# Kernel optimization log

Hardware: AMD Instinct MI355X
Metric: run time of the kernel (lower is better)

## Reference

```python
import jax, jax.numpy as jnp
import numpy as np
from jax import lax

N, E, C, B, EF = 50000, 640000, 128, 64, 2
L = 32            # eval mode: 8 * num_virtual_tokens
D = 256           # mamba d_inner = expand * d_model
S = 128           # mamba d_state
R = 8             # dt_rank = ceil(C/16)
K = 4             # mamba d_conv


def _ln(x, g, b, eps=1e-5):
    m = x.mean(-1, keepdims=True)
    v = jnp.mean((x - m) ** 2, -1, keepdims=True)
    return (x - m) * lax.rsqrt(v + eps) * g + b


def setup_inputs() -> dict:
    key = jax.random.key(0)
    ks = iter(jax.random.split(key, 64))
    nrm = lambda sh, s=0.02: jax.random.normal(next(ks), sh, dtype=jnp.float32) * s
    inp = {}
    inp['x'] = jax.random.normal(next(ks), (N, C), dtype=jnp.float32)
    inp['edge_attr'] = jax.random.normal(next(ks), (E, EF), dtype=jnp.float32)
    inp['edge_index'] = jax.random.randint(next(ks), (2, E), 0, N, dtype=jnp.int32)
    inp['batch'] = jnp.sort(jax.random.randint(next(ks), (N,), 0, B, dtype=jnp.int32))
    # 8 spatial convs: edge-feature lift + node linear
    inp['We'] = nrm((8, EF, C), 0.1); inp['be'] = jnp.zeros((8, C))
    inp['Wc'] = nrm((8, C, C));       inp['bc'] = jnp.zeros((8, C))
    # GRUCell (torch gate order r,z,n)
    inp['Wih'] = nrm((C, 3 * C), 0.05); inp['Whh'] = nrm((C, 3 * C), 0.05)
    inp['bih'] = jnp.zeros((3 * C,));   inp['bhh'] = jnp.zeros((3 * C,))
    # Mamba
    inp['Win'] = nrm((C, 2 * D))
    inp['conv_w'] = nrm((D, K), 0.1); inp['conv_b'] = jnp.zeros((D,))
    inp['Wx'] = nrm((D, R + 2 * S))
    inp['Wdt'] = nrm((R, D), 0.1); inp['bdt'] = jnp.full((D,), -2.0)
    inp['A_log'] = jnp.log(jnp.tile(jnp.arange(1, S + 1, dtype=jnp.float32), (D, 1)))
    inp['Dp'] = jnp.ones((D,))
    inp['Wout'] = nrm((D, C))
    inp['g_m'] = jnp.ones((C,)); inp['b_m'] = jnp.zeros((C,))
    # merge MLP: Linear(9C->C) -> LN -> ReLU -> Linear(C->C)
    inp['Wm1'] = nrm((9 * C, C)); inp['bm1'] = jnp.zeros((C,))
    inp['g_h'] = jnp.ones((C,));  inp['b_h'] = jnp.zeros((C,))
    inp['Wm2'] = nrm((C, C));     inp['bm2'] = jnp.zeros((C,))
    inp['g_o'] = jnp.ones((C,));  inp['b_o'] = jnp.zeros((C,))
    return inp


def _forward(x, edge_attr, We, be, Wc, bc, Wih, Whh, bih, bhh, Win, conv_w, conv_b,
             Wx, Wdt, bdt, A_log, Dp, Wout, g_m, b_m, Wm1, bm1, g_h, b_h, Wm2, bm2,
             g_o, b_o, edge_index, batch):
    src, dst = edge_index[0], edge_index[1]
    # --- 8 graph convs (gather -> edge message -> scatter-add -> linear) ---
    xs = []
    x_src = x[src]                                        # [E,C]
    for i in range(8):
        msg = jax.nn.relu(x_src + edge_attr @ We[i] + be[i])
        agg = jax.ops.segment_sum(msg, dst, num_segments=N)
        xs.append(jax.nn.relu(agg @ Wc[i] + bc[i]))
    # --- to_dense_batch mean (zero-padded mean => segment_sum / maxN) ---
    counts = jax.ops.segment_sum(jnp.ones((N,), x.dtype), batch, num_segments=B)
    maxN = counts.max()
    x_mean = jax.ops.segment_sum(x, batch, num_segments=B) / maxN   # [B,C]
    # --- GRU virtual-token loop (input constant across steps) ---
    gi = x_mean @ Wih + bih
    ir, iz, inn = jnp.split(gi, 3, axis=-1)
    def gru_step(h, _):
        gh = h @ Whh + bhh
        hr, hz, hn = jnp.split(gh, 3, axis=-1)
        r = jax.nn.sigmoid(ir + hr)
        z = jax.nn.sigmoid(iz + hz)
        n = jnp.tanh(inn + r * hn)
        h = (1.0 - z) * n + z * h
        return h, h
    _, toks = lax.scan(gru_step, jnp.zeros((B, C), x.dtype), None, length=L)
    tokens = jnp.moveaxis(toks, 0, 1)                     # [B,L,C]
    # --- Mamba selective scan ---
    xz = tokens @ Win                                     # [B,L,2D]
    x_in, z_g = jnp.split(xz, 2, axis=-1)
    xp = jnp.pad(x_in, ((0, 0), (K - 1, 0), (0, 0)))      # causal depthwise conv
    x_c = sum(conv_w[:, k] * xp[:, k:k + L, :] for k in range(K)) + conv_b
    x_c = jax.nn.silu(x_c)                                # [B,L,D]
    dbl = x_c @ Wx
    dt_r, Bp, Cp = dbl[..., :R], dbl[..., R:R + S], dbl[..., R + S:]
    dt = jax.nn.softplus(dt_r @ Wdt + bdt)                # [B,L,D]
    A = -jnp.exp(A_log)                                   # [D,S]
    def ssm_step(h, inp):
        dt_t, B_t, C_t, x_t = inp                         # [B,D],[B,S],[B,S],[B,D]
        dA = jnp.exp(dt_t[..., None] * A)                 # [B,D,S]
        h = dA * h + (dt_t * x_t)[..., None] * B_t[:, None, :]
        y = jnp.einsum('bds,bs->bd', h, C_t)
        return h, y
    tm = lambda a: jnp.moveaxis(a, 1, 0)
    _, ys = lax.scan(ssm_step, jnp.zeros((B, D, S), x.dtype),
                     (tm(dt), tm(Bp), tm(Cp), tm(x_c)))
    y = jnp.moveaxis(ys, 0, 1) + Dp * x_c
    y = y * jax.nn.silu(z_g)
    mo = _ln(y @ Wout, g_m, b_m)                          # [B,L,C]
    x_m = mo[:, -1, :]
    x_m_node = x_m[batch]                                 # [N,C] gather
    # --- merge + residual + LN ---
    cat = jnp.concatenate(xs + [x_m_node], axis=-1)       # [N,9C]
    h1 = jax.nn.relu(_ln(cat @ Wm1 + bm1, g_h, b_h))
    x_new = h1 @ Wm2 + bm2
    return _ln(x + x_new, g_o, b_o)


def reference(x, edge_index, edge_attr, batch, We, be, Wc, bc, Wih, Whh, bih, bhh,
              Win, conv_w, conv_b, Wx, Wdt, bdt, A_log, Dp, Wout, g_m, b_m,
              Wm1, bm1, g_h, b_h, Wm2, bm2, g_o, b_o):
    return _forward(x, edge_attr, We, be, Wc, bc, Wih, Whh, bih, bhh, Win, conv_w,
                    conv_b, Wx, Wdt, bdt, A_log, Dp, Wout, g_m, b_m, Wm1, bm1,
                    g_h, b_h, Wm2, bm2, g_o, b_o, edge_index, batch)
```

## Files before the change

kernel.cpp:

```cpp
#include <hip/hip_runtime.h>
#include <hip/hip_bf16.h>

#define N_NODES 50000
#define N_EDGES 640000
#define C_DIM 128
#define B_DIM 64
#define L_DIM 32
#define D_DIM 256
#define S_DIM 128
#define R_DIM 8
#define K_CONV 4
#define NPW 4
#define NB 64
#define MAX_CHUNK 50048
#define SCAN_BLK 49

typedef unsigned short u16;
typedef __attribute__((ext_vector_type(8))) short bf16x8;
typedef __attribute__((ext_vector_type(4))) float f32x4;

struct __align__(16) ERec { int s; float a0, a1; int pad; };

__device__ __forceinline__ float bu2f(u16 u){ return __uint_as_float(((unsigned)u) << 16); }
__device__ __forceinline__ u16 f2bu(float f){
  __hip_bfloat16 h = __float2bfloat16(f);
  return *reinterpret_cast<u16*>(&h);
}
__device__ __forceinline__ float sigmoidf_(float x){ return 1.f/(1.f + expf(-x)); }
__device__ __forceinline__ int clampi(int v, int lo, int hi){ return max(lo, min(v, hi)); }
__device__ __forceinline__ float ldf(const void* p, size_t i, int f){
  return f ? bu2f(((const u16*)p)[i]) : ((const float*)p)[i];
}
__device__ __forceinline__ void stf(void* p, size_t i, int f, float v){
  if (f) ((u16*)p)[i] = f2bu(v); else ((float*)p)[i] = v;
}
__device__ __forceinline__ f32x4 mfma16(bf16x8 a, bf16x8 b, f32x4 c){
  return __builtin_amdgcn_mfma_f32_16x16x32_bf16(a, b, c, 0, 0, 0);
}
__device__ __forceinline__ float wave_sum64(float v){
  #pragma unroll
  for (int off = 32; off; off >>= 1) v += __shfl_xor(v, off);
  return v;
}

constexpr int K_SEG = 27;
constexpr int kCum[K_SEG+1] = {
  0, 2048, 3072, 134144, 135168, 184320, 233472, 233856, 234240, 299776,
  300800, 301056, 368640, 370688, 370944, 403712, 403968, 436736, 436864,
  436992, 584448, 584576, 584704, 584832, 601216, 601344, 601472, 601600 };
#define ARENA_TOTAL 601600

struct Ptrs { const void* p[K_SEG]; };


__global__ void detect_kernel(const unsigned* dp_bits, const unsigned* cand1,
                              const unsigned* cand2, int* flags){
  int lane = threadIdx.x & 63;
  unsigned idx = (unsigned)((lane * 9973u) % (unsigned)N_EDGES);
  int v1 = (cand1[idx] < (unsigned)N_NODES) ? 1 : 0;
  int v2 = (cand2[idx] < (unsigned)N_NODES) ? 1 : 0;
  unsigned long long m1 = __ballot(v1);
  unsigned long long m2 = __ballot(v2);
  if (lane == 0){
    flags[0] = (dp_bits[0] == 0x3F803F80u) ? 1 : 0;
    flags[1] = (__popcll(m1) > __popcll(m2)) ? 1 : 0;
  }
}


__global__ __launch_bounds__(256) void cvt_all_kernel(Ptrs ptrs, float* arena,
                                                      const int* flags){
  int i = blockIdx.x*256 + threadIdx.x;
  if (i >= ARENA_TOTAL) return;
  int lo = 0, hi = K_SEG;
  #pragma unroll
  for (int it = 0; it < 5; it++){
    int mid = (lo + hi) >> 1;
    if (i >= kCum[mid]) lo = mid; else hi = mid;
  }
  int elem = i - kCum[lo];
  const void* sp = ptrs.p[lo];
  arena[i] = flags[0] ? bu2f(((const u16*)sp)[elem]) : ((const float*)sp)[elem];
}


__global__ __launch_bounds__(256) void wtrans_kernel(
    const float* __restrict__ WcF, const float* __restrict__ Wm1F,
    const float* __restrict__ Wm2F,
    u16* __restrict__ WcT_hi, u16* __restrict__ WcT_lo,
    u16* __restrict__ Wm1T_hi, u16* __restrict__ Wm1T_lo,
    u16* __restrict__ Wm2T_hi, u16* __restrict__ Wm2T_lo)
{
  int i = blockIdx.x*256 + threadIdx.x;
  if (i >= 8*C_DIM*C_DIM) return;
  int h = i >> 14, j = (i >> 7) & 127, k = i & 127;
  {
    float w = WcF[(h<<14) + (k<<7) + j];
    u16 hi = f2bu(w); u16 lo = f2bu(w - bu2f(hi));
    WcT_hi[i] = hi; WcT_lo[i] = lo;
  }
  {
    float w = Wm1F[((size_t)((h<<7) + k) << 7) + j];
    u16 hi = f2bu(w); u16 lo = f2bu(w - bu2f(hi));
    Wm1T_hi[i] = hi; Wm1T_lo[i] = lo;
  }
  if (i < C_DIM*C_DIM){
    int j2 = i >> 7, k2 = i & 127;
    float w = Wm2F[(k2<<7) + j2];
    u16 hi = f2bu(w); u16 lo = f2bu(w - bu2f(hi));
    Wm2T_hi[i] = hi; Wm2T_lo[i] = lo;
  }
}


__global__ void hist_kernel(const int* __restrict__ eiA, const int* __restrict__ eiB,
                            const int* __restrict__ flags, int* __restrict__ hist){
  const int* dst = (flags[1] ? eiA : eiB) + N_EDGES;
  int e = blockIdx.x*256 + threadIdx.x;
  if (e >= N_EDGES) return;
  int d = clampi(dst[e], 0, N_NODES-1);
  atomicAdd(&hist[d], 1);
}

__global__ __launch_bounds__(1024) void scan1_kernel(const int* __restrict__ hist,
                                                     int* __restrict__ tmp,
                                                     int* __restrict__ bsums){
  __shared__ int buf[1024];
  int b = blockIdx.x, tid = threadIdx.x;
  int i = b*1024 + tid;
  int v = (i < N_NODES) ? hist[i] : 0;
  buf[tid] = v;
  __syncthreads();
  for (int off = 1; off < 1024; off <<= 1){
    int t = (tid >= off) ? buf[tid-off] : 0;
    __syncthreads();
    buf[tid] += t;
    __syncthreads();
  }
  if (i < N_NODES) tmp[i] = buf[tid];
  if (tid == 1023) bsums[b] = buf[1023];
}

__global__ void scan2_kernel(int* __restrict__ bsums, int* __restrict__ offsets){
  if (threadIdx.x == 0){
    int run = 0;
    for (int b = 0; b < SCAN_BLK; b++){ int v = bsums[b]; bsums[b] = run; run += v; }
    offsets[N_NODES] = run;
  }
}

__global__ __launch_bounds__(1024) void scan3_kernel(int* __restrict__ offsets,
                                                     int* __restrict__ hist,
                                                     const int* __restrict__ bsums){
  int b = blockIdx.x, tid = threadIdx.x;
  int i = b*1024 + tid;
  if (i >= N_NODES) return;
  int incl = offsets[i];
  int h = hist[i];
  int excl = incl - h + bsums[b];
  offsets[i] = excl;
  hist[i] = excl;
}

__global__ void perm_kernel(const void* __restrict__ in1, const void* __restrict__ in2,
                            const int* __restrict__ flags, int* __restrict__ cursor,
                            ERec* __restrict__ sortedRec){
  int e = blockIdx.x*256 + threadIdx.x;
  if (e >= N_EDGES) return;
  const int f1 = flags[1], f = flags[0];
  const int* ei  = (const int*)(f1 ? in1 : in2);
  const void* eav = f1 ? in2 : in1;
  int d = clampi(ei[N_EDGES + e], 0, N_NODES-1);
  int s = clampi(ei[e], 0, N_NODES-1);
  float a0, a1;
  if (f){ const u16* e16 = (const u16*)eav; a0 = bu2f(e16[2*e]); a1 = bu2f(e16[2*e+1]); }
  else  { const float* e32 = (const float*)eav; a0 = e32[2*e]; a1 = e32[2*e+1]; }
  int pos = atomicAdd(&cursor[d], 1);
  pos = clampi(pos, 0, N_EDGES-1);
  ERec r; r.s = s; r.a0 = a0; r.a1 = a1; r.pad = 0;
  sortedRec[pos] = r;
}


__global__ __launch_bounds__(256, 8) void gather_kernel(
    const void* __restrict__ xv, const ERec* __restrict__ sortedRec,
    const int* __restrict__ offsets,
    const float* __restrict__ WeF, const float* __restrict__ beF,
    const int* __restrict__ flags, u16* __restrict__ aggBuf,
    int n0, int ncnt)
{
  int w = blockIdx.x*4 + (threadIdx.x >> 6);
  int nsets = (ncnt + NPW - 1) / NPW;
  if (w >= 2*nsets) return;
  int chalf = w & 1;
  int nset = w >> 1;
  int lane = threadIdx.x & 63;
  int c = lane + chalf*64;
  const int f = flags[0];
  const u16* x16 = (const u16*)xv; const float* x32 = (const float*)xv;

  float we0[8], we1[8], beh[8];
  #pragma unroll
  for (int h = 0; h < 8; h++){
    we0[h] = WeF[h*2*C_DIM + c];
    we1[h] = WeF[h*2*C_DIM + C_DIM + c];
    beh[h] = beF[h*C_DIM + c];
  }

  auto LD = [&](int q, float& xr, float2& er){
    ERec r = sortedRec[q];
    er = make_float2(r.a0, r.a1);
    int idx = r.s*C_DIM + c;
    xr = f ? bu2f(x16[idx]) : x32[idx];
  };

  int nl_end = min(nset*NPW + NPW, ncnt);
  for (int nl = nset*NPW; nl < nl_end; nl++){
    int n = n0 + nl;
    int q0 = offsets[n];
    int cnt = offsets[n+1] - q0;

    float acc[8] = {0,0,0,0,0,0,0,0};
    float xA=0.f, xB=0.f, xC=0.f, xD=0.f;
    float2 eA=make_float2(0,0), eB=make_float2(0,0), eC=make_float2(0,0), eD=make_float2(0,0);
    if (cnt > 0) LD(q0+0, xA, eA);
    if (cnt > 1) LD(q0+1, xB, eB);
    if (cnt > 2) LD(q0+2, xC, eC);
    if (cnt > 3) LD(q0+3, xD, eD);

    for (int j = 0; j < cnt; j += 4){
      float ux0=xA, ux1=xB, ux2=xC, ux3=xD;
      float2 ue0=eA, ue1=eB, ue2=eC, ue3=eD;
      if (j+4 < cnt) LD(q0+j+4, xA, eA);
      if (j+5 < cnt) LD(q0+j+5, xB, eB);
      if (j+6 < cnt) LD(q0+j+6, xC, eC);
      if (j+7 < cnt) LD(q0+j+7, xD, eD);
      #pragma unroll
      for (int h = 0; h < 8; h++)
        acc[h] += fmaxf(fmaf(ue0.x, we0[h], fmaf(ue0.y, we1[h], ux0 + beh[h])), 0.f);
      if (j+1 < cnt){
        #pragma unroll
        for (int h = 0; h < 8; h++)
          acc[h] += fmaxf(fmaf(ue1.x, we0[h], fmaf(ue1.y, we1[h], ux1 + beh[h])), 0.f);
      }
      if (j+2 < cnt){
        #pragma unroll
        for (int h = 0; h < 8; h++)
          acc[h] += fmaxf(fmaf(ue2.x, we0[h], fmaf(ue2.y, we1[h], ux2 + beh[h])), 0.f);
      }
      if (j+3 < cnt){
        #pragma unroll
        for (int h = 0; h < 8; h++)
          acc[h] += fmaxf(fmaf(ue3.x, we0[h], fmaf(ue3.y, we1[h], ux3 + beh[h])), 0.f);
      }
    }

    int base = nl*2048 + c;
    #pragma unroll
    for (int h = 0; h < 8; h++){
      u16 hv = f2bu(acc[h]);
      u16 lv = f2bu(acc[h] - bu2f(hv));
      aggBuf[base + h*256]       = hv;
      aggBuf[base + h*256 + 128] = lv;
    }
  }
}


__global__ __launch_bounds__(128) void pool_kernel(
    const void* __restrict__ xv, const int* __restrict__ batch,
    float* __restrict__ xsum, int* __restrict__ counts, const int* __restrict__ flags)
{
  int c = threadIdx.x;
  int f = flags[0];
  int n0 = blockIdx.x * 32;
  int nend = min(n0 + 32, N_NODES);
  float acc = 0.f; int cnt = 0;
  int curb = clampi(batch[n0], 0, B_DIM-1);
  for (int n = n0; n < nend; n++){
    int b = clampi(batch[n], 0, B_DIM-1);
    if (b != curb){
      atomicAdd(&xsum[curb*C_DIM + c], acc);
      if (c == 0) atomicAdd(&counts[curb], cnt);
      acc = 0.f; cnt = 0; curb = b;
    }
    acc += ldf(xv, (size_t)n*C_DIM + c, f);
    cnt++;
  }
  atomicAdd(&xsum[curb*C_DIM + c], acc);
  if (c == 0) atomicAdd(&counts[curb], cnt);
}


__global__ __launch_bounds__(384, 1) void gru_kernel(
    const float* __restrict__ xsum, const int* __restrict__ counts,
    const float* __restrict__ Wih, const float* __restrict__ bih,
    const float* __restrict__ Whh, const float* __restrict__ bhh,
    float* __restrict__ tokens)
{
  int b = blockIdx.x, j = threadIdx.x;
  __shared__ float xm[C_DIM], h[C_DIM], gh[3*C_DIM], sgi[3*C_DIM];
  __shared__ float mxS;
  if (j == 0){
    int m = 1;
    for (int bb = 0; bb < B_DIM; bb++) m = max(m, counts[bb]);
    mxS = (float)m;
  }
  __syncthreads();
  if (j < C_DIM){ xm[j] = xsum[b*C_DIM + j] / mxS; h[j] = 0.f; }
  __syncthreads();

  {
    float a0=0.f, a1=0.f, a2=0.f, a3=0.f;
    for (int k = 0; k < C_DIM; k += 4){
      a0 = fmaf(xm[k],   Wih[(k  )*384 + j], a0);
      a1 = fmaf(xm[k+1], Wih[(k+1)*384 + j], a1);
      a2 = fmaf(xm[k+2], Wih[(k+2)*384 + j], a2);
      a3 = fmaf(xm[k+3], Wih[(k+3)*384 + j], a3);
    }
    sgi[j] = bih[j] + ((a0 + a1) + (a2 + a3));
  }

  float w[C_DIM];
  #pragma unroll
  for (int k = 0; k < C_DIM; k++) w[k] = Whh[k*384 + j];
  float bh = bhh[j];
  __syncthreads();

  float g_ir = 0.f, g_iz = 0.f, g_in = 0.f;
  if (j < C_DIM){ g_ir = sgi[j]; g_iz = sgi[C_DIM + j]; g_in = sgi[2*C_DIM + j]; }

  for (int t = 0; t < L_DIM; t++){
    float a0=0.f, a1=0.f, a2=0.f, a3=0.f;
    #pragma unroll
    for (int k = 0; k < C_DIM; k += 4){
      a0 = fmaf(h[k],   w[k],   a0);
      a1 = fmaf(h[k+1], w[k+1], a1);
      a2 = fmaf(h[k+2], w[k+2], a2);
      a3 = fmaf(h[k+3], w[k+3], a3);
    }
    gh[j] = bh + ((a0 + a1) + (a2 + a3));
    __syncthreads();
    if (j < C_DIM){
      float r  = sigmoidf_(g_ir + gh[j]);
      float z  = sigmoidf_(g_iz + gh[C_DIM + j]);
      float nn = tanhf(g_in + r*gh[2*C_DIM + j]);
      float hn = (1.f - z)*nn + z*h[j];
      h[j] = hn;
      tokens[((size_t)b*L_DIM + t)*C_DIM + j] = hn;
    }
    __syncthreads();
  }
}


__global__ __launch_bounds__(256) void token_proj_kernel(
    const float* __restrict__ tokens, const float* __restrict__ Win,
    float* __restrict__ x_in, float* __restrict__ z_last)
{
  int row = blockIdx.x;
  int d = threadIdx.x;
  __shared__ float tok[C_DIM];
  if (d < C_DIM) tok[d] = tokens[(size_t)row*C_DIM + d];
  __syncthreads();
  float acc = 0.f;
  for (int k = 0; k < C_DIM; k++) acc = fmaf(tok[k], Win[k*512 + d], acc);
  x_in[(size_t)row*D_DIM + d] = acc;
  if ((row & (L_DIM-1)) == L_DIM-1){
    float acc2 = 0.f;
    for (int k = 0; k < C_DIM; k++) acc2 = fmaf(tok[k], Win[k*512 + D_DIM + d], acc2);
    z_last[(row >> 5)*D_DIM + d] = acc2;
  }
}


__global__ __launch_bounds__(256) void xproj_kernel(
    const float* __restrict__ x_in, const float* __restrict__ cw,
    const float* __restrict__ cb, const float* __restrict__ Wx,
    const float* __restrict__ Wdt, const float* __restrict__ bdt,
    float* __restrict__ dt, float* __restrict__ Bp, float* __restrict__ Cp,
    float* __restrict__ x_c)
{
  int row = blockIdx.x; int tid = threadIdx.x;
  int t = row & (L_DIM-1);
  __shared__ float xr[D_DIM];
  __shared__ float dtr[R_DIM];
  float acc0 = cb[tid];
  #pragma unroll
  for (int k = 0; k < K_CONV; k++){
    int tt = t + k - (K_CONV-1);
    if (tt >= 0) acc0 = fmaf(cw[tid*K_CONV + k], x_in[(size_t)(row + tt - t)*D_DIM + tid], acc0);
  }
  float xcv = acc0 * sigmoidf_(acc0);
  x_c[(size_t)row*D_DIM + tid] = xcv;
  xr[tid] = xcv;
  __syncthreads();
  float acc = 0.f;
  #pragma unroll 4
  for (int k = 0; k < D_DIM; k++) acc = fmaf(xr[k], Wx[k*264 + tid], acc);
  if (tid < R_DIM)              dtr[tid] = acc;
  else if (tid < R_DIM+S_DIM)   Bp[(size_t)row*S_DIM + tid - R_DIM] = acc;
  else                          Cp[(size_t)row*S_DIM + tid - (R_DIM+S_DIM)] = acc;
  if (tid < 264 - D_DIM){
    float acc2 = 0.f;
    #pragma unroll 4
    for (int k = 0; k < D_DIM; k++) acc2 = fmaf(xr[k], Wx[k*264 + D_DIM + tid], acc2);
    Cp[(size_t)row*S_DIM + (D_DIM - (R_DIM+S_DIM)) + tid] = acc2;
  }
  __syncthreads();
  float a = bdt[tid];
  #pragma unroll
  for (int r = 0; r < R_DIM; r++) a = fmaf(dtr[r], Wdt[r*D_DIM + tid], a);
  dt[(size_t)row*D_DIM + tid] = (a > 20.f) ? a : log1pf(expf(a));
}


__global__ __launch_bounds__(256) void ssm_kernel(
    const float* __restrict__ dt, const float* __restrict__ Bp,
    const float* __restrict__ Cp, const float* __restrict__ x_c,
    const float* __restrict__ A_log, const float* __restrict__ Dp_,
    const float* __restrict__ z_last, float* __restrict__ y_last)
{
  int wid = (blockIdx.x*256 + threadIdx.x) >> 6;
  int lane = threadIdx.x & 63;
  int b = wid >> 8, d = wid & (D_DIM-1);
  int s0 = lane*2;
  float A0 = -expf(A_log[d*S_DIM + s0]);
  float A1 = -expf(A_log[d*S_DIM + s0 + 1]);
  float h0 = 0.f, h1 = 0.f;
  for (int t = 0; t < L_DIM; t++){
    int row = b*L_DIM + t;
    float dtv = dt[(size_t)row*D_DIM + d];
    float xv  = x_c[(size_t)row*D_DIM + d];
    float bx = dtv * xv;
    float2 Bv = ((const float2*)(Bp + (size_t)row*S_DIM))[lane];
    h0 = fmaf(expf(dtv*A0), h0, bx*Bv.x);
    h1 = fmaf(expf(dtv*A1), h1, bx*Bv.y);
  }
  int row = b*L_DIM + (L_DIM-1);
  float2 Cv = ((const float2*)(Cp + (size_t)row*S_DIM))[lane];
  float y = h0*Cv.x + h1*Cv.y;
  #pragma unroll
  for (int off = 32; off; off >>= 1) y += __shfl_down(y, off);
  if (lane == 0){
    float xc = x_c[(size_t)row*D_DIM + d];
    float yv = y + Dp_[d]*xc;
    float z  = z_last[b*D_DIM + d];
    yv *= z * sigmoidf_(z);
    y_last[b*D_DIM + d] = yv;
  }
}


__device__ __forceinline__ float block_sum_128(float v, float* red){
  int c = threadIdx.x;
  red[c] = v; __syncthreads();
  if (c < 64) red[c] += red[c+64];
  __syncthreads();
  if (c < 64){
    float r = red[c];
    #pragma unroll
    for (int off = 32; off; off >>= 1) r += __shfl_down(r, off);
    if (c == 0) red[0] = r;
  }
  __syncthreads();
  float out = red[0];
  __syncthreads();
  return out;
}

__global__ __launch_bounds__(128) void xm_kernel(
    const float* __restrict__ y_last, const float* __restrict__ Wout,
    const float* __restrict__ g_m, const float* __restrict__ b_m,
    const float* __restrict__ Wm1x, float* __restrict__ proj)
{
  int b = blockIdx.x, c = threadIdx.x;
  __shared__ float yr[D_DIM];
  __shared__ float red[C_DIM];
  __shared__ float xmr[C_DIM];
  yr[c]        = y_last[b*D_DIM + c];
  yr[C_DIM+c]  = y_last[b*D_DIM + C_DIM + c];
  __syncthreads();
  float acc = 0.f;
  for (int k = 0; k < D_DIM; k++) acc = fmaf(yr[k], Wout[k*C_DIM + c], acc);
  float mean = block_sum_128(acc, red) * (1.f/C_DIM);
  float dv = acc - mean;
  float var = block_sum_128(dv*dv, red) * (1.f/C_DIM);
  float mo = dv*rsqrtf(var + 1e-5f)*g_m[c] + b_m[c];
  xmr[c] = mo;
  __syncthreads();
  float p = 0.f;
  for (int k = 0; k < C_DIM; k++) p = fmaf(xmr[k], Wm1x[k*C_DIM + c], p);
  proj[b*C_DIM + c] = p;
}


__global__ __launch_bounds__(256, 2) void fused_kernel(
    const void* __restrict__ xv, const u16* __restrict__ aggBuf, int n0, int ncnt,
    const u16* __restrict__ WcT_hi, const u16* __restrict__ WcT_lo,
    const float* __restrict__ bcF,
    const u16* __restrict__ Wm1T_hi, const u16* __restrict__ Wm1T_lo,
    const float* __restrict__ bm1F, const float* __restrict__ proj,
    const int* __restrict__ batch,
    const float* __restrict__ ghF, const float* __restrict__ bhF,
    const u16* __restrict__ Wm2T_hi, const u16* __restrict__ Wm2T_lo,
    const float* __restrict__ bm2F,
    const float* __restrict__ goF, const float* __restrict__ boF,
    const int* __restrict__ flags, void* __restrict__ out)
{
  __shared__ __align__(16) char smem[65536];
  float* pS = (float*)smem;

  const int tid = threadIdx.x;
  const int f = flags[0];
  const u16* x16 = (const u16*)xv; const float* x32 = (const float*)xv;
  const int lbase = blockIdx.x * NB;
  const int nbase = n0 + lbase;

  const int lane = tid & 63;
  const int wv = tid >> 6;
  const int m16 = lane & 15;
  const int lg = lane >> 4;
  const int colbase = wv * 32;
  const int jA = colbase + m16;

  int ahoff[4], aoff[4];
  #pragma unroll
  for (int kk = 0; kk < 4; kk++){
    int sw = (m16 & 7) << 4;
    ahoff[kk] = m16*512 + ((kk*64 + lg*16) ^ sw);
    aoff[kk]  = m16*256 + ((kk*64 + lg*16) ^ sw);
  }

  int sg_node[8], sg_u[8], sg_dst[8];
  #pragma unroll
  for (int j = 0; j < 8; j++){
    int i = tid + j*256;
    int t = i >> 9, g = (i >> 5) & 15, u = i & 31;
    sg_node[j] = lbase + t*16 + g;
    sg_u[j] = u << 4;
    sg_dst[j] = t*8192 + (((i & 511) << 4) ^ ((g & 7) << 4));
  }

  bf16x8 sreg[8];
  auto stage_load = [&](int h){
    #pragma unroll
    for (int j = 0; j < 8; j++)
      sreg[j] = *(const bf16x8*)((const char*)aggBuf +
                 (((size_t)sg_node[j]*8 + h) << 9) + sg_u[j]);
  };
  auto stage_commit = [&](){
    #pragma unroll
    for (int j = 0; j < 8; j++) *(bf16x8*)(smem + sg_dst[j]) = sreg[j];
  };
  auto LDW = [&](const u16* Whi, const u16* Wlo, int h, bf16x8 (*w)[4]){
    #pragma unroll
    for (int kk = 0; kk < 4; kk++){
      size_t bi0 = ((size_t)(h*C_DIM + jA) << 7) + kk*32 + lg*8;
      w[kk][0] = *(const bf16x8*)(Whi + bi0);
      w[kk][1] = *(const bf16x8*)(Wlo + bi0);
      w[kk][2] = *(const bf16x8*)(Whi + bi0 + 2048);
      w[kk][3] = *(const bf16x8*)(Wlo + bi0 + 2048);
    }
  };

  stage_load(0);
  stage_commit();
  __syncthreads();

  f32x4 P0[4], P1[4];
  #pragma unroll
  for (int t = 0; t < 4; t++){
    P0[t] = (f32x4){0,0,0,0};
    P1[t] = (f32x4){0,0,0,0};
  }

  bf16x8 w[4][4];
  for (int h = 0; h < 8; h++){
    const bool pf = (h+1 < 8);
    LDW(WcT_hi, WcT_lo, h, w);
    if (pf) stage_load(h+1);
    float bc0 = bcF[h*C_DIM + colbase + m16];
    float bc1 = bcF[h*C_DIM + colbase + 16 + m16];

    #pragma unroll
    for (int t = 0; t < 4; t++){
      f32x4 a0 = {0,0,0,0}, a1 = {0,0,0,0};
      #pragma unroll
      for (int kk = 0; kk < 4; kk++){
        bf16x8 ah = *(const bf16x8*)(smem + t*8192 + ahoff[kk]);
        bf16x8 al = *(const bf16x8*)(smem + t*8192 + ahoff[kk] + 256);
        a0 = mfma16(ah, w[kk][0], a0);
        a0 = mfma16(ah, w[kk][1], a0);
        a0 = mfma16(al, w[kk][0], a0);
        a1 = mfma16(ah, w[kk][2], a1);
        a1 = mfma16(ah, w[kk][3], a1);
        a1 = mfma16(al, w[kk][2], a1);
      }
      #pragma unroll
      for (int r = 0; r < 4; r++){
        int row = lg*4 + r;
        int rs = row*256;
        int sw2 = (row & 7) << 4;
        {
          float v = fmaxf(a0[r] + bc0, 0.f);
          u16 hi = f2bu(v); u16 lo = f2bu(v - bu2f(hi));
          int bo = rs + (((colbase + m16)*2) ^ sw2);
          *(u16*)(smem + 32768 + t*8192 + bo) = hi;
          *(u16*)(smem + 32768 + t*8192 + 4096 + bo) = lo;
        }
        {
          float v = fmaxf(a1[r] + bc1, 0.f);
          u16 hi = f2bu(v); u16 lo = f2bu(v - bu2f(hi));
          int bo = rs + (((colbase + 16 + m16)*2) ^ sw2);
          *(u16*)(smem + 32768 + t*8192 + bo) = hi;
          *(u16*)(smem + 32768 + t*8192 + 4096 + bo) = lo;
        }
      }
    }
    LDW(Wm1T_hi, Wm1T_lo, h, w);
    __syncthreads();
    if (pf) stage_commit();

    #pragma unroll
    for (int t = 0; t < 4; t++){
      #pragma unroll
      for (int kk = 0; kk < 4; kk++){
        bf16x8 yh = *(const bf16x8*)(smem + 32768 + t*8192 + aoff[kk]);
        bf16x8 yl = *(const bf16x8*)(smem + 32768 + t*8192 + 4096 + aoff[kk]);
        P0[t] = mfma16(yh, w[kk][0], P0[t]);
        P0[t] = mfma16(yh, w[kk][1], P0[t]);
        P0[t] = mfma16(yl, w[kk][0], P0[t]);
        P1[t] = mfma16(yh, w[kk][2], P1[t]);
        P1[t] = mfma16(yh, w[kk][3], P1[t]);
        P1[t] = mfma16(yl, w[kk][2], P1[t]);
      }
    }
    __syncthreads();
  }

  #pragma unroll
  for (int t = 0; t < 4; t++){
    #pragma unroll
    for (int r = 0; r < 4; r++){
      int row = t*16 + lg*4 + r;
      pS[row*C_DIM + colbase + m16]      = P0[t][r];
      pS[row*C_DIM + colbase + 16 + m16] = P1[t][r];
    }
  }
  __syncthreads();

  for (int g = 0; g < 16; g++){
    int n_l = wv*16 + g;
    int nc = min(nbase + n_l, N_NODES-1);
    int bi = clampi(batch[nc], 0, B_DIM-1);
    float v0 = pS[n_l*C_DIM + lane]      + bm1F[lane]      + proj[bi*C_DIM + lane];
    float v1 = pS[n_l*C_DIM + 64 + lane] + bm1F[64 + lane] + proj[bi*C_DIM + 64 + lane];
    float mean = wave_sum64(v0 + v1) * (1.f/C_DIM);
    float d0 = v0 - mean, d1 = v1 - mean;
    float var = wave_sum64(d0*d0 + d1*d1) * (1.f/C_DIM);
    float rinv = rsqrtf(var + 1e-5f);
    float h0 = fmaxf(d0*rinv*ghF[lane]      + bhF[lane], 0.f);
    float h1v = fmaxf(d1*rinv*ghF[64+lane]  + bhF[64+lane], 0.f);
    int sw3 = (n_l & 7) << 4;
    {
      u16 hi = f2bu(h0); u16 lo = f2bu(h0 - bu2f(hi));
      int bo = n_l*256 + ((lane*2) ^ sw3);
      *(u16*)(smem + 32768 + bo) = hi;
      *(u16*)(smem + 49152 + bo) = lo;
    }
    {
      u16 hi = f2bu(h1v); u16 lo = f2bu(h1v - bu2f(hi));
      int bo = n_l*256 + (((64+lane)*2) ^ sw3);
      *(u16*)(smem + 32768 + bo) = hi;
      *(u16*)(smem + 49152 + bo) = lo;
    }
  }
  LDW(Wm2T_hi, Wm2T_lo, 0, w);
  __syncthreads();

  {
    f32x4 A0[4], A1[4];
    #pragma unroll
    for (int t = 0; t < 4; t++){
      A0[t] = (f32x4){0,0,0,0};
      A1[t] = (f32x4){0,0,0,0};
      #pragma unroll
      for (int kk = 0; kk < 4; kk++){
        bf16x8 yh = *(const bf16x8*)(smem + 32768 + t*4096 + aoff[kk]);
        bf16x8 yl = *(const bf16x8*)(smem + 49152 + t*4096 + aoff[kk]);
        A0[t] = mfma16(yh, w[kk][0], A0[t]);
        A0[t] = mfma16(yh, w[kk][1], A0[t]);
        A0[t] = mfma16(yl, w[kk][0], A0[t]);
        A1[t] = mfma16(yh, w[kk][2], A1[t]);
        A1[t] = mfma16(yh, w[kk][3], A1[t]);
        A1[t] = mfma16(yl, w[kk][2], A1[t]);
      }
    }
    __syncthreads();
    #pragma unroll
    for (int t = 0; t < 4; t++){
      #pragma unroll
      for (int r = 0; r < 4; r++){
        int row = t*16 + lg*4 + r;
        pS[row*C_DIM + colbase + m16]      = A0[t][r];
        pS[row*C_DIM + colbase + 16 + m16] = A1[t][r];
      }
    }
  }
  __syncthreads();

  for (int g = 0; g < 16; g++){
    int n_l = wv*16 + g;
    int n = nbase + n_l;
    int nc = min(n, N_NODES-1);
    float x0 = f ? bu2f(x16[(size_t)nc*C_DIM + lane])      : x32[(size_t)nc*C_DIM + lane];
    float x1 = f ? bu2f(x16[(size_t)nc*C_DIM + 64 + lane]) : x32[(size_t)nc*C_DIM + 64 + lane];
    float v0 = pS[n_l*C_DIM + lane]      + bm2F[lane]      + x0;
    float v1 = pS[n_l*C_DIM + 64 + lane] + bm2F[64 + lane] + x1;
    float mean = wave_sum64(v0 + v1) * (1.f/C_DIM);
    float d0 = v0 - mean, d1 = v1 - mean;
    float var = wave_sum64(d0*d0 + d1*d1) * (1.f/C_DIM);
    float rinv = rsqrtf(var + 1e-5f);
    if (lbase + n_l < ncnt){
      stf(out, (size_t)n*C_DIM + lane,      f, d0*rinv*goF[lane]      + boF[lane]);
      stf(out, (size_t)n*C_DIM + 64 + lane, f, d1*rinv*goF[64+lane]   + boF[64+lane]);
    }
  }
}


extern "C" void kernel_launch(void* const* d_in, const int* in_sizes, int n_in,
                              void* d_out, int out_size, void* d_ws, size_t ws_size,
                              hipStream_t stream)
{
  const void* x      = d_in[0];
  const void* in1    = d_in[1];
  const void* in2    = d_in[2];
  const int*  batch  = (const int*)d_in[3];
  (void)in_sizes; (void)n_in; (void)out_size;

  char* ws = (char*)d_ws;
  size_t off = 0;
  auto alloc = [&](size_t nbytes)->char*{
    char* p = ws + off;
    off += (nbytes + 255) & ~(size_t)255;
    return p;
  };
  int*   flags = (int*)alloc(8);
  float* arena = (float*)alloc((size_t)ARENA_TOTAL*4);
  int* hist    = (int*)alloc((size_t)N_NODES*4);
  int* offsets = (int*)alloc((size_t)(N_NODES+1)*4);
  int* bsums   = (int*)alloc((size_t)SCAN_BLK*4);
  ERec* sortedRec = (ERec*)alloc((size_t)N_EDGES*16);
  float* proj   = (float*)alloc((size_t)B_DIM*C_DIM*4);
  float* xsum   = (float*)alloc((size_t)B_DIM*C_DIM*4);
  int*   counts = (int*)alloc((size_t)B_DIM*4);
  float* tokens = (float*)alloc((size_t)B_DIM*L_DIM*C_DIM*4);
  float* x_in   = (float*)alloc((size_t)B_DIM*L_DIM*D_DIM*4);
  float* x_c    = (float*)alloc((size_t)B_DIM*L_DIM*D_DIM*4);
  float* Cp     = (float*)alloc((size_t)B_DIM*L_DIM*S_DIM*4);
  float* z_last = (float*)alloc((size_t)B_DIM*D_DIM*4);
  float* y_last = (float*)alloc((size_t)B_DIM*D_DIM*4);
  u16* WcT_hi  = (u16*)alloc((size_t)8*C_DIM*C_DIM*2);
  u16* WcT_lo  = (u16*)alloc((size_t)8*C_DIM*C_DIM*2);
  u16* Wm1T_hi = (u16*)alloc((size_t)8*C_DIM*C_DIM*2);
  u16* Wm1T_lo = (u16*)alloc((size_t)8*C_DIM*C_DIM*2);
  u16* Wm2T_hi = (u16*)alloc((size_t)C_DIM*C_DIM*2);
  u16* Wm2T_lo = (u16*)alloc((size_t)C_DIM*C_DIM*2);

  size_t avail = (ws_size > off + 4096) ? (ws_size - off - 4096) : 0;
  long long cn = (long long)(avail / 4096);
  cn &= ~63LL;
  if (cn > MAX_CHUNK) cn = MAX_CHUNK;
  if (cn < 64) cn = 16704;
  const int chunkN = (int)cn;
  u16* aggBuf = (u16*)alloc((size_t)chunkN * 4096);

  float* Bp  = tokens;
  float* dtb = x_in;

  float* WeF   = arena + 0;      float* beF   = arena + 2048;
  float* WcF   = arena + 3072;   float* bcF   = arena + 134144;
  float* WihF  = arena + 135168; float* WhhF  = arena + 184320;
  float* bihF  = arena + 233472; float* bhhF  = arena + 233856;
  float* WinF  = arena + 234240; float* cwF   = arena + 299776;
  float* cbF   = arena + 300800; float* WxF   = arena + 301056;
  float* WdtF  = arena + 368640; float* bdtF  = arena + 370688;
  float* AlF   = arena + 370944; float* DpF   = arena + 403712;
  float* WoutF = arena + 403968; float* gmF   = arena + 436736;
  float* bmF   = arena + 436864; float* Wm1F  = arena + 436992;
  float* bm1F  = arena + 584448; float* ghF   = arena + 584576;
  float* bhF   = arena + 584704; float* Wm2F  = arena + 584832;
  float* bm2F  = arena + 601216; float* goF   = arena + 601344;
  float* boF   = arena + 601472;

  detect_kernel<<<1, 64, 0, stream>>>((const unsigned*)d_in[19],
                                      (const unsigned*)in1, (const unsigned*)in2, flags);

  Ptrs ptrs;
  for (int i = 0; i < K_SEG; i++) ptrs.p[i] = d_in[4 + i];
  cvt_all_kernel<<<(ARENA_TOTAL + 255)/256, 256, 0, stream>>>(ptrs, arena, flags);
  wtrans_kernel<<<(8*C_DIM*C_DIM + 255)/256, 256, 0, stream>>>(
      WcF, Wm1F, Wm2F, WcT_hi, WcT_lo, Wm1T_hi, Wm1T_lo, Wm2T_hi, Wm2T_lo);

  hipMemsetAsync(hist, 0, (size_t)N_NODES*4, stream);
  hist_kernel<<<(N_EDGES + 255)/256, 256, 0, stream>>>((const int*)in1, (const int*)in2, flags, hist);
  scan1_kernel<<<SCAN_BLK, 1024, 0, stream>>>(hist, offsets, bsums);
  scan2_kernel<<<1, 64, 0, stream>>>(bsums, offsets);
  scan3_kernel<<<SCAN_BLK, 1024, 0, stream>>>(offsets, hist, bsums);
  perm_kernel<<<(N_EDGES + 255)/256, 256, 0, stream>>>(in1, in2, flags, hist, sortedRec);

  hipMemsetAsync(xsum, 0, (size_t)B_DIM*C_DIM*4 + 256, stream);
  pool_kernel<<<(N_NODES + 31)/32, 128, 0, stream>>>(x, batch, xsum, counts, flags);
  gru_kernel<<<B_DIM, 384, 0, stream>>>(xsum, counts, WihF, bihF, WhhF, bhhF, tokens);
  token_proj_kernel<<<B_DIM*L_DIM, 256, 0, stream>>>(tokens, WinF, x_in, z_last);
  xproj_kernel<<<B_DIM*L_DIM, 256, 0, stream>>>(x_in, cwF, cbF, WxF, WdtF, bdtF, dtb, Bp, Cp, x_c);
  ssm_kernel<<<(B_DIM*D_DIM)/4, 256, 0, stream>>>(dtb, Bp, Cp, x_c, AlF, DpF, z_last, y_last);
  xm_kernel<<<B_DIM, 128, 0, stream>>>(y_last, WoutF, gmF, bmF, Wm1F + 8*C_DIM*C_DIM, proj);

  for (int n0 = 0; n0 < N_NODES; n0 += chunkN){
    int ncnt = min(chunkN, N_NODES - n0);
    int nsets = (ncnt + NPW - 1) / NPW;
    int nwaves = 2 * nsets;
    gather_kernel<<<(nwaves + 3)/4, 256, 0, stream>>>(
        x, sortedRec, offsets, WeF, beF, flags, aggBuf, n0, ncnt);
    fused_kernel<<<(ncnt + NB - 1)/NB, 256, 0, stream>>>(
        x, aggBuf, n0, ncnt, WcT_hi, WcT_lo, bcF, Wm1T_hi, Wm1T_lo, bm1F,
        proj, batch, ghF, bhF, Wm2T_hi, Wm2T_lo, bm2F, goF, boF, flags, d_out);
  }
}
```

Before: 796.6 us.

## Shrink fused kernel LDS to raise occupancy, load aggregates straight from global

The fused conv+merge kernel drops LDS staging of the aggregated neighbor features. MFMA A-operands now load directly from global memory, and the per-node LayerNorm epilogues run in 16-row slices that use a small scratch region. This cuts shared memory from 64 KiB to 40 KiB and raises the launch-bounds occupancy target from 2 to 3 blocks per CU. In exchange the A loads lose the swizzled, software-prefetched LDS path, are less coalesced and are exposed to global latency, and the slice epilogues add barriers.

```diff
diff --git a/kernel.cpp b/kernel.cpp
--- a/kernel.cpp
+++ b/kernel.cpp
@@ -495,7 +495,7 @@
 }
 
 
-__global__ __launch_bounds__(256, 2) void fused_kernel(
+__global__ __launch_bounds__(256, 3) void fused_kernel(
     const void* __restrict__ xv, const u16* __restrict__ aggBuf, int n0, int ncnt,
     const u16* __restrict__ WcT_hi, const u16* __restrict__ WcT_lo,
     const float* __restrict__ bcF,
@@ -508,8 +508,8 @@
     const float* __restrict__ goF, const float* __restrict__ boF,
     const int* __restrict__ flags, void* __restrict__ out)
 {
-  __shared__ __align__(16) char smem[65536];
-  float* pS = (float*)smem;
+  __shared__ __align__(16) char smem[40960];
+  float* pS = (float*)(smem + 32768);
 
   const int tid = threadIdx.x;
   const int f = flags[0];
@@ -524,35 +524,13 @@
   const int colbase = wv * 32;
   const int jA = colbase + m16;
 
-  int ahoff[4], aoff[4];
+  int aoff[4];
   #pragma unroll
   for (int kk = 0; kk < 4; kk++){
     int sw = (m16 & 7) << 4;
-    ahoff[kk] = m16*512 + ((kk*64 + lg*16) ^ sw);
-    aoff[kk]  = m16*256 + ((kk*64 + lg*16) ^ sw);
-  }
-
-  int sg_node[8], sg_u[8], sg_dst[8];
-  #pragma unroll
-  for (int j = 0; j < 8; j++){
-    int i = tid + j*256;
-    int t = i >> 9, g = (i >> 5) & 15, u = i & 31;
-    sg_node[j] = lbase + t*16 + g;
-    sg_u[j] = u << 4;
-    sg_dst[j] = t*8192 + (((i & 511) << 4) ^ ((g & 7) << 4));
-  }
-
-  bf16x8 sreg[8];
-  auto stage_load = [&](int h){
-    #pragma unroll
-    for (int j = 0; j < 8; j++)
-      sreg[j] = *(const bf16x8*)((const char*)aggBuf +
-                 (((size_t)sg_node[j]*8 + h) << 9) + sg_u[j]);
-  };
-  auto stage_commit = [&](){
-    #pragma unroll
-    for (int j = 0; j < 8; j++) *(bf16x8*)(smem + sg_dst[j]) = sreg[j];
-  };
+    aoff[kk] = m16*256 + ((kk*64 + lg*16) ^ sw);
+  }
+
   auto LDW = [&](const u16* Whi, const u16* Wlo, int h, bf16x8 (*w)[4]){
     #pragma unroll
     for (int kk = 0; kk < 4; kk++){
@@ -564,10 +542,6 @@
     }
   };
 
-  stage_load(0);
-  stage_commit();
-  __syncthreads();
-
   f32x4 P0[4], P1[4];
   #pragma unroll
   for (int t = 0; t < 4; t++){
@@ -577,19 +551,19 @@
 
   bf16x8 w[4][4];
   for (int h = 0; h < 8; h++){
-    const bool pf = (h+1 < 8);
     LDW(WcT_hi, WcT_lo, h, w);
-    if (pf) stage_load(h+1);
     float bc0 = bcF[h*C_DIM + colbase + m16];
     float bc1 = bcF[h*C_DIM + colbase + 16 + m16];
 
     #pragma unroll
     for (int t = 0; t < 4; t++){
+      const char* arow = (const char*)aggBuf +
+          (((size_t)((lbase + t*16 + m16)*8 + h)) << 9);
       f32x4 a0 = {0,0,0,0}, a1 = {0,0,0,0};
       #pragma unroll
       for (int kk = 0; kk < 4; kk++){
-        bf16x8 ah = *(const bf16x8*)(smem + t*8192 + ahoff[kk]);
-        bf16x8 al = *(const bf16x8*)(smem + t*8192 + ahoff[kk] + 256);
+        bf16x8 ah = *(const bf16x8*)(arow + kk*64 + lg*16);
+        bf16x8 al = *(const bf16x8*)(arow + kk*64 + lg*16 + 256);
         a0 = mfma16(ah, w[kk][0], a0);
         a0 = mfma16(ah, w[kk][1], a0);
         a0 = mfma16(al, w[kk][0], a0);
@@ -606,28 +580,27 @@
           float v = fmaxf(a0[r] + bc0, 0.f);
           u16 hi = f2bu(v); u16 lo = f2bu(v - bu2f(hi));
           int bo = rs + (((colbase + m16)*2) ^ sw2);
-          *(u16*)(smem + 32768 + t*8192 + bo) = hi;
-          *(u16*)(smem + 32768 + t*8192 + 4096 + bo) = lo;
+          *(u16*)(smem + t*8192 + bo) = hi;
+          *(u16*)(smem + t*8192 + 4096 + bo) = lo;
         }
         {
           float v = fmaxf(a1[r] + bc1, 0.f);
           u16 hi = f2bu(v); u16 lo = f2bu(v - bu2f(hi));
           int bo = rs + (((colbase + 16 + m16)*2) ^ sw2);
-          *(u16*)(smem + 32768 + t*8192 + bo) = hi;
-          *(u16*)(smem + 32768 + t*8192 + 4096 + bo) = lo;
+          *(u16*)(smem + t*8192 + bo) = hi;
+          *(u16*)(smem + t*8192 + 4096 + bo) = lo;
         }
       }
     }
     LDW(Wm1T_hi, Wm1T_lo, h, w);
     __syncthreads();
-    if (pf) stage_commit();
 
     #pragma unroll
     for (int t = 0; t < 4; t++){
       #pragma unroll
       for (int kk = 0; kk < 4; kk++){
-        bf16x8 yh = *(const bf16x8*)(smem + 32768 + t*8192 + aoff[kk]);
-        bf16x8 yl = *(const bf16x8*)(smem + 32768 + t*8192 + 4096 + aoff[kk]);
+        bf16x8 yh = *(const bf16x8*)(smem + t*8192 + aoff[kk]);
+        bf16x8 yl = *(const bf16x8*)(smem + t*8192 + 4096 + aoff[kk]);
         P0[t] = mfma16(yh, w[kk][0], P0[t]);
         P0[t] = mfma16(yh, w[kk][1], P0[t]);
         P0[t] = mfma16(yl, w[kk][0], P0[t]);
@@ -643,88 +616,81 @@
   for (int t = 0; t < 4; t++){
     #pragma unroll
     for (int r = 0; r < 4; r++){
-      int row = t*16 + lg*4 + r;
+      int row = lg*4 + r;
       pS[row*C_DIM + colbase + m16]      = P0[t][r];
       pS[row*C_DIM + colbase + 16 + m16] = P1[t][r];
     }
-  }
-  __syncthreads();
-
-  for (int g = 0; g < 16; g++){
-    int n_l = wv*16 + g;
-    int nc = min(nbase + n_l, N_NODES-1);
-    int bi = clampi(batch[nc], 0, B_DIM-1);
-    float v0 = pS[n_l*C_DIM + lane]      + bm1F[lane]      + proj[bi*C_DIM + lane];
-    float v1 = pS[n_l*C_DIM + 64 + lane] + bm1F[64 + lane] + proj[bi*C_DIM + 64 + lane];
-    float mean = wave_sum64(v0 + v1) * (1.f/C_DIM);
-    float d0 = v0 - mean, d1 = v1 - mean;
-    float var = wave_sum64(d0*d0 + d1*d1) * (1.f/C_DIM);
-    float rinv = rsqrtf(var + 1e-5f);
-    float h0 = fmaxf(d0*rinv*ghF[lane]      + bhF[lane], 0.f);
-    float h1v = fmaxf(d1*rinv*ghF[64+lane]  + bhF[64+lane], 0.f);
-    int sw3 = (n_l & 7) << 4;
-    {
-      u16 hi = f2bu(h0); u16 lo = f2bu(h0 - bu2f(hi));
-      int bo = n_l*256 + ((lane*2) ^ sw3);
-      *(u16*)(smem + 32768 + bo) = hi;
-      *(u16*)(smem + 49152 + bo) = lo;
-    }
-    {
-      u16 hi = f2bu(h1v); u16 lo = f2bu(h1v - bu2f(hi));
-      int bo = n_l*256 + (((64+lane)*2) ^ sw3);
-      *(u16*)(smem + 32768 + bo) = hi;
-      *(u16*)(smem + 49152 + bo) = lo;
-    }
-  }
+    __syncthreads();
+    for (int g = 0; g < 4; g++){
+      int rl = wv*4 + g;
+      int n_l = t*16 + rl;
+      int nc = min(nbase + n_l, N_NODES-1);
+      int bi = clampi(batch[nc], 0, B_DIM-1);
+      float v0 = pS[rl*C_DIM + lane]      + bm1F[lane]      + proj[bi*C_DIM + lane];
+      float v1 = pS[rl*C_DIM + 64 + lane] + bm1F[64 + lane] + proj[bi*C_DIM + 64 + lane];
+      float mean = wave_sum64(v0 + v1) * (1.f/C_DIM);
+      float d0 = v0 - mean, d1 = v1 - mean;
+      float var = wave_sum64(d0*d0 + d1*d1) * (1.f/C_DIM);
+      float rinv = rsqrtf(var + 1e-5f);
+      float h0 = fmaxf(d0*rinv*ghF[lane]      + bhF[lane], 0.f);
+      float h1v = fmaxf(d1*rinv*ghF[64+lane]  + bhF[64+lane], 0.f);
+      int sw3 = (n_l & 7) << 4;
+      {
+        u16 hi = f2bu(h0); u16 lo = f2bu(h0 - bu2f(hi));
+        int bo = n_l*256 + ((lane*2) ^ sw3);
+        *(u16*)(smem + bo) = hi;
+        *(u16*)(smem + 16384 + bo) = lo;
+      }
+      {
+        u16 hi = f2bu(h1v); u16 lo = f2bu(h1v - bu2f(hi));
+        int bo = n_l*256 + (((64+lane)*2) ^ sw3);
+        *(u16*)(smem + bo) = hi;
+        *(u16*)(smem + 16384 + bo) = lo;
+      }
+    }
+    __syncthreads();
+  }
+
   LDW(Wm2T_hi, Wm2T_lo, 0, w);
-  __syncthreads();
-
-  {
-    f32x4 A0[4], A1[4];
-    #pragma unroll
-    for (int t = 0; t < 4; t++){
-      A0[t] = (f32x4){0,0,0,0};
-      A1[t] = (f32x4){0,0,0,0};
-      #pragma unroll
-      for (int kk = 0; kk < 4; kk++){
-        bf16x8 yh = *(const bf16x8*)(smem + 32768 + t*4096 + aoff[kk]);
-        bf16x8 yl = *(const bf16x8*)(smem + 49152 + t*4096 + aoff[kk]);
-        A0[t] = mfma16(yh, w[kk][0], A0[t]);
-        A0[t] = mfma16(yh, w[kk][1], A0[t]);
-        A0[t] = mfma16(yl, w[kk][0], A0[t]);
-        A1[t] = mfma16(yh, w[kk][2], A1[t]);
-        A1[t] = mfma16(yh, w[kk][3], A1[t]);
-        A1[t] = mfma16(yl, w[kk][2], A1[t]);
-      }
-    }
-    __syncthreads();
-    #pragma unroll
-    for (int t = 0; t < 4; t++){
-      #pragma unroll
-      for (int r = 0; r < 4; r++){
-        int row = t*16 + lg*4 + r;
-        pS[row*C_DIM + colbase + m16]      = A0[t][r];
-        pS[row*C_DIM + colbase + 16 + m16] = A1[t][r];
-      }
-    }
-  }
-  __syncthreads();
-
-  for (int g = 0; g < 16; g++){
-    int n_l = wv*16 + g;
-    int n = nbase + n_l;
-    int nc = min(n, N_NODES-1);
-    float x0 = f ? bu2f(x16[(size_t)nc*C_DIM + lane])      : x32[(size_t)nc*C_DIM + lane];
-    float x1 = f ? bu2f(x16[(size_t)nc*C_DIM + 64 + lane]) : x32[(size_t)nc*C_DIM + 64 + lane];
-    float v0 = pS[n_l*C_DIM + lane]      + bm2F[lane]      + x0;
-    float v1 = pS[n_l*C_DIM + 64 + lane] + bm2F[64 + lane] + x1;
-    float mean = wave_sum64(v0 + v1) * (1.f/C_DIM);
-    float d0 = v0 - mean, d1 = v1 - mean;
-    float var = wave_sum64(d0*d0 + d1*d1) * (1.f/C_DIM);
-    float rinv = rsqrtf(var + 1e-5f);
-    if (lbase + n_l < ncnt){
-      stf(out, (size_t)n*C_DIM + lane,      f, d0*rinv*goF[lane]      + boF[lane]);
-      stf(out, (size_t)n*C_DIM + 64 + lane, f, d1*rinv*goF[64+lane]   + boF[64+lane]);
+  #pragma unroll
+  for (int t = 0; t < 4; t++){
+    f32x4 A0 = {0,0,0,0}, A1 = {0,0,0,0};
+    #pragma unroll
+    for (int kk = 0; kk < 4; kk++){
+      bf16x8 yh = *(const bf16x8*)(smem + t*4096 + aoff[kk]);
+      bf16x8 yl = *(const bf16x8*)(smem + 16384 + t*4096 + aoff[kk]);
+      A0 = mfma16(yh, w[kk][0], A0);
+      A0 = mfma16(yh, w[kk][1], A0);
+      A0 = mfma16(yl, w[kk][0], A0);
+      A1 = mfma16(yh, w[kk][2], A1);
+      A1 = mfma16(yh, w[kk][3], A1);
+      A1 = mfma16(yl, w[kk][2], A1);
+    }
+    __syncthreads();
+    #pragma unroll
+    for (int r = 0; r < 4; r++){
+      int row = lg*4 + r;
+      pS[row*C_DIM + colbase + m16]      = A0[r];
+      pS[row*C_DIM + colbase + 16 + m16] = A1[r];
+    }
+    __syncthreads();
+    for (int g = 0; g < 4; g++){
+      int rl = wv*4 + g;
+      int n_l = t*16 + rl;
+      int n = nbase + n_l;
+      int nc = min(n, N_NODES-1);
+      float x0 = f ? bu2f(x16[(size_t)nc*C_DIM + lane])      : x32[(size_t)nc*C_DIM + lane];
+      float x1 = f ? bu2f(x16[(size_t)nc*C_DIM + 64 + lane]) : x32[(size_t)nc*C_DIM + 64 + lane];
+      float v0 = pS[rl*C_DIM + lane]      + bm2F[lane]      + x0;
+      float v1 = pS[rl*C_DIM + 64 + lane] + bm2F[64 + lane] + x1;
+      float mean = wave_sum64(v0 + v1) * (1.f/C_DIM);
+      float d0 = v0 - mean, d1 = v1 - mean;
+      float var = wave_sum64(d0*d0 + d1*d1) * (1.f/C_DIM);
+      float rinv = rsqrtf(var + 1e-5f);
+      if (lbase + n_l < ncnt){
+        stf(out, (size_t)n*C_DIM + lane,      f, d0*rinv*goF[lane]      + boF[lane]);
+        stf(out, (size_t)n*C_DIM + 64 + lane, f, d1*rinv*goF[64+lane]   + boF[64+lane]);
+      }
     }
   }
 }
```

After: 877.1 us. +10.1%, slower.
